# Kernel optimization log

Measured on AMD Instinct MI355X. Metric: run time of the kernel, lower is better.

The kernel has to match this reference:

```python
import jax, jax.numpy as jnp
import numpy as np

DIM = 1024
NUM_HEADS = 16
HEAD_DIM = DIM // NUM_HEADS
SCALE = 1.0 / float(np.sqrt(HEAD_DIM))


def setup_inputs() -> dict:
    key = jax.random.key(0)
    ks = jax.random.split(key, 5)
    B, S = 2, 2048
    x = jax.random.normal(ks[0], (B, S, DIM), dtype=jnp.float32)
    qkv_w = jax.random.normal(ks[1], (3 * DIM, DIM), dtype=jnp.float32) * (1.0 / np.sqrt(DIM))
    qkv_b = jax.random.normal(ks[2], (3 * DIM,), dtype=jnp.float32) * 0.02
    proj_w = jax.random.normal(ks[3], (DIM, DIM), dtype=jnp.float32) * (1.0 / np.sqrt(DIM))
    proj_b = jax.random.normal(ks[4], (DIM,), dtype=jnp.float32) * 0.02
    return {"x": x, "qkv_w": qkv_w, "qkv_b": qkv_b, "proj_w": proj_w, "proj_b": proj_b}


def reference(x, qkv_w, qkv_b, proj_w, proj_b):
    B, S, _ = x.shape
    # qkv projection: (B,S,3*DIM) -> (3, B, H, S, Dh)
    qkv = x @ qkv_w.T + qkv_b
    qkv = qkv.reshape(B, S, 3, NUM_HEADS, HEAD_DIM).transpose(2, 0, 3, 1, 4)
    q, k, v = qkv[0], qkv[1], qkv[2]
    # scaled dot-product attention (full score matrix, as in the original)
    scores = jnp.einsum('bhqd,bhkd->bhqk', q, k) * SCALE
    attn = jax.nn.softmax(scores, axis=-1)
    out = jnp.einsum('bhqk,bhkd->bhqd', attn, v)  # (B,H,S,Dh)
    out = out.transpose(0, 2, 1, 3).reshape(B, S, DIM)
    return out @ proj_w.T + proj_b
```

## Files before the change

### kernel.cpp

```cpp
#include <hip/hip_runtime.h>

#define DIM_ 1024
#define NH_ 16
#define HD_ 64
#define B_ 2
#define S_ 2048
#define M_ (B_ * S_)
#define NQKV_ (3 * DIM_)

typedef __attribute__((ext_vector_type(8))) __bf16 bf16x8;
typedef __attribute__((ext_vector_type(4))) __bf16 bf16x4;
typedef __attribute__((ext_vector_type(4))) float f32x4;

__device__ __forceinline__ void gl_lds16(const void* g, void* l) {
  __builtin_amdgcn_global_load_lds(
      (__attribute__((address_space(1))) void*)const_cast<void*>(g),
      (__attribute__((address_space(3))) void*)l, 16, 0, 0);
}

#define N4_X 1048576
#define N4_W1 786432
#define N4_W2 262144
__global__ __launch_bounds__(256) void cast_all(const float* __restrict__ x,
                                                const float* __restrict__ w1,
                                                const float* __restrict__ w2,
                                                __bf16* __restrict__ xb,
                                                __bf16* __restrict__ w1b,
                                                __bf16* __restrict__ w2b) {
  int i = blockIdx.x * 256 + threadIdx.x;
  const int stride = gridDim.x * 256;
  for (; i < N4_X + N4_W1 + N4_W2; i += stride) {
    const float4* src;
    bf16x4* dst;
    int j;
    if (i < N4_X) { src = (const float4*)x; dst = (bf16x4*)xb; j = i; }
    else if (i < N4_X + N4_W1) { src = (const float4*)w1; dst = (bf16x4*)w1b; j = i - N4_X; }
    else { src = (const float4*)w2; dst = (bf16x4*)w2b; j = i - (N4_X + N4_W1); }
    float4 v = src[j];
    bf16x4 o;
    o[0] = (__bf16)v.x; o[1] = (__bf16)v.y; o[2] = (__bf16)v.z; o[3] = (__bf16)v.w;
    dst[j] = o;
  }
}

template <int MODE>
__global__ __launch_bounds__(256) void gemm_bt(const __bf16* __restrict__ A,
                                               const __bf16* __restrict__ Bw,
                                               const float* __restrict__ bias,
                                               __bf16* __restrict__ Qp, __bf16* __restrict__ Kp,
                                               __bf16* __restrict__ Vt, float* __restrict__ Cout) {
  constexpr int KD = 1024;
  __shared__ __bf16 As[128 * 64];
  __shared__ __bf16 Bs[128 * 64];
  const int tid = threadIdx.x;
  const int lane = tid & 63;
  const int wave = tid >> 6;
  const int quad = lane >> 4;
  const int r16 = lane & 15;
  const int wm = wave >> 1;
  const int wn = wave & 1;
  const int m0 = blockIdx.y * 128;
  const int n0 = blockIdx.x * 128;

  const f32x4 fz = {0.f, 0.f, 0.f, 0.f};
  f32x4 acc[4][4];
#pragma unroll
  for (int i = 0; i < 4; ++i)
#pragma unroll
    for (int j = 0; j < 4; ++j) acc[i][j] = fz;

  const __bf16* ga[4];
  const __bf16* gb[4];
  __bf16 *la[4], *lb[4];
#pragma unroll
  for (int i = 0; i < 4; ++i) {
    const int c = tid + i * 256;
    const int r = c >> 3, cc = c & 7;
    const int col = ((cc ^ (r & 7)) * 8);
    ga[i] = A + (size_t)(m0 + r) * KD + col;
    gb[i] = Bw + (size_t)(n0 + r) * KD + col;
    la[i] = &As[c * 8];
    lb[i] = &Bs[c * 8];
  }

  for (int kt = 0; kt < KD / 64; ++kt) {
    __syncthreads();
#pragma unroll
    for (int i = 0; i < 4; ++i) {
      gl_lds16(ga[i], la[i]); ga[i] += 64;
      gl_lds16(gb[i], lb[i]); gb[i] += 64;
    }
    __syncthreads();

    bf16x8 af[2][4], bfr[2][4];
#pragma unroll
    for (int sub = 0; sub < 2; ++sub) {
      const int ch = ((sub * 4 + quad) ^ (r16 & 7)) * 8;
#pragma unroll
      for (int mt = 0; mt < 4; ++mt)
        af[sub][mt] = *(const bf16x8*)&As[(wm * 64 + mt * 16 + r16) * 64 + ch];
#pragma unroll
      for (int nt = 0; nt < 4; ++nt)
        bfr[sub][nt] = *(const bf16x8*)&Bs[(wn * 64 + nt * 16 + r16) * 64 + ch];
    }
#pragma unroll
    for (int sub = 0; sub < 2; ++sub)
#pragma unroll
      for (int mt = 0; mt < 4; ++mt)
#pragma unroll
        for (int nt = 0; nt < 4; ++nt)
          acc[mt][nt] =
              __builtin_amdgcn_mfma_f32_16x16x32_bf16(af[sub][mt], bfr[sub][nt], acc[mt][nt], 0, 0, 0);
  }

  if (MODE == 0) {
#pragma unroll
    for (int nt = 0; nt < 4; ++nt) {
      const int n = n0 + wn * 64 + nt * 16 + r16;
      const int sel = n >> 10;
      const int h = (n >> 6) & 15;
      const int dh = n & 63;
      const float bs = bias[n];
      if (sel == 2) {
#pragma unroll
        for (int mt = 0; mt < 4; ++mt) {
          const int m = m0 + wm * 64 + mt * 16 + quad * 4;
          const int b = m >> 11;
          const int s = m & 2047;
          const int slot = (s & ~31) | (((s >> 2) & 3) << 3) | (((s >> 4) & 1) << 2);
          bf16x4 ov;
#pragma unroll
          for (int r = 0; r < 4; ++r) ov[r] = (__bf16)(acc[mt][nt][r] + bs);
          *(bf16x4*)&Vt[((size_t)((b * NH_ + h) * HD_ + dh)) * S_ + slot] = ov;
        }
      } else {
        __bf16* dst = (sel == 0) ? Qp : Kp;
        const float mul = (sel == 0) ? 0.18033688011112042f : 1.0f;
#pragma unroll
        for (int mt = 0; mt < 4; ++mt) {
#pragma unroll
          for (int r = 0; r < 4; ++r) {
            const int m = m0 + wm * 64 + mt * 16 + quad * 4 + r;
            const int b = m >> 11;
            const int s = m & 2047;
            dst[((size_t)((b * NH_ + h) * S_ + s)) * HD_ + dh] =
                (__bf16)((acc[mt][nt][r] + bs) * mul);
          }
        }
      }
    }
  } else {
#pragma unroll
    for (int nt = 0; nt < 4; ++nt) {
      const int n = n0 + wn * 64 + nt * 16 + r16;
      const float bs = bias[n];
#pragma unroll
      for (int mt = 0; mt < 4; ++mt) {
#pragma unroll
        for (int r = 0; r < 4; ++r) {
          const int m = m0 + wm * 64 + mt * 16 + quad * 4 + r;
          Cout[(size_t)m * DIM_ + n] = acc[mt][nt][r] + bs;
        }
      }
    }
  }
}

__global__ __launch_bounds__(256) void attn(const __bf16* __restrict__ Qp,
                                            const __bf16* __restrict__ Kp,
                                            const __bf16* __restrict__ Vtp,
                                            __bf16* __restrict__ ctx) {
  __shared__ __bf16 Ks[128 * 64];
  __shared__ __bf16 Vs[64 * 128];
  const int tid = threadIdx.x;
  const int lane = tid & 63;
  const int wave = tid >> 6;
  const int quad = lane >> 4;
  const int r16 = lane & 15;
  const int bh = blockIdx.y;
  const int q0 = blockIdx.x * 128;

  bf16x8 qf[2][2];
#pragma unroll
  for (int g = 0; g < 2; ++g) {
    const __bf16* qb = Qp + ((size_t)bh * S_ + q0 + wave * 32 + g * 16 + r16) * HD_;
    qf[g][0] = *(const bf16x8*)(qb + quad * 8);
    qf[g][1] = *(const bf16x8*)(qb + 32 + quad * 8);
  }

  const f32x4 fz = {0.f, 0.f, 0.f, 0.f};
  f32x4 o[2][4];
  float lsum[2] = {0.f, 0.f};
#pragma unroll
  for (int g = 0; g < 2; ++g)
#pragma unroll
    for (int d = 0; d < 4; ++d) o[g][d] = fz;

  const __bf16* gk[4];
  const __bf16* gv[4];
  __bf16 *lk[4], *lv[4];
#pragma unroll
  for (int i = 0; i < 4; ++i) {
    int c = tid + i * 256;
    int kr = c >> 3, kc = c & 7;
    gk[i] = Kp + ((size_t)bh * S_ + kr) * HD_ + ((kc ^ (kr & 7)) * 8);
    lk[i] = &Ks[c * 8];
    int vr = c >> 4, vc = c & 15;
    gv[i] = Vtp + ((size_t)bh * HD_ + vr) * S_ + ((vc ^ (vr & 15)) * 8);
    lv[i] = &Vs[c * 8];
  }

  for (int kt = 0; kt < S_ / 128; ++kt) {
    __syncthreads();
#pragma unroll
    for (int i = 0; i < 4; ++i) { gl_lds16(gk[i], lk[i]); gk[i] += 128 * HD_; }
#pragma unroll
    for (int i = 0; i < 4; ++i) { gl_lds16(gv[i], lv[i]); gv[i] += 128; }
    __syncthreads();

    f32x4 sa[2][8];
#pragma unroll
    for (int mt = 0; mt < 8; ++mt) {
      const int row = mt * 16 + r16;
      bf16x8 k0 = *(const bf16x8*)&Ks[row * 64 + ((quad ^ (row & 7)) * 8)];
      bf16x8 k1 = *(const bf16x8*)&Ks[row * 64 + (((4 + quad) ^ (row & 7)) * 8)];
#pragma unroll
      for (int g = 0; g < 2; ++g) {
        f32x4 t = fz;
        t = __builtin_amdgcn_mfma_f32_16x16x32_bf16(k0, qf[g][0], t, 0, 0, 0);
        t = __builtin_amdgcn_mfma_f32_16x16x32_bf16(k1, qf[g][1], t, 0, 0, 0);
        sa[g][mt] = t;
      }
    }

    bf16x8 pf[2][4];
#pragma unroll
    for (int g = 0; g < 2; ++g)
#pragma unroll
      for (int ks = 0; ks < 4; ++ks)
#pragma unroll
        for (int r = 0; r < 4; ++r) {
          float p0 = __builtin_amdgcn_exp2f(sa[g][2 * ks][r]);
          float p1 = __builtin_amdgcn_exp2f(sa[g][2 * ks + 1][r]);
          lsum[g] += p0 + p1;
          pf[g][ks][r] = (__bf16)p0;
          pf[g][ks][4 + r] = (__bf16)p1;
        }

#pragma unroll
    for (int ks = 0; ks < 4; ++ks)
#pragma unroll
      for (int dt = 0; dt < 4; ++dt) {
        const int row = dt * 16 + r16;
        bf16x8 va = *(const bf16x8*)&Vs[row * 128 + (((4 * ks + quad) ^ (row & 15)) * 8)];
#pragma unroll
        for (int g = 0; g < 2; ++g)
          o[g][dt] = __builtin_amdgcn_mfma_f32_16x16x32_bf16(va, pf[g][ks], o[g][dt], 0, 0, 0);
      }
  }

  const int b = bh >> 4, h = bh & 15;
#pragma unroll
  for (int g = 0; g < 2; ++g) {
    float l = lsum[g];
    l += __shfl_xor(l, 16);
    l += __shfl_xor(l, 32);
    const float inv = 1.0f / l;
    const int s = q0 + wave * 32 + g * 16 + r16;
#pragma unroll
    for (int dt = 0; dt < 4; ++dt) {
      bf16x4 ov;
#pragma unroll
      for (int r = 0; r < 4; ++r) ov[r] = (__bf16)(o[g][dt][r] * inv);
      *(bf16x4*)&ctx[((size_t)(b * S_ + s)) * DIM_ + h * 64 + dt * 16 + quad * 4] = ov;
    }
  }
}

extern "C" void kernel_launch(void* const* d_in, const int* in_sizes, int n_in, void* d_out,
                              int out_size, void* d_ws, size_t ws_size, hipStream_t stream) {
  const float* x = (const float*)d_in[0];
  const float* qkv_w = (const float*)d_in[1];
  const float* qkv_b = (const float*)d_in[2];
  const float* proj_w = (const float*)d_in[3];
  const float* proj_b = (const float*)d_in[4];
  float* out = (float*)d_out;

  char* ws = (char*)d_ws;
  __bf16* Xb = (__bf16*)(ws);
  __bf16* Wb = (__bf16*)(ws + 8388608);
  __bf16* Pb = (__bf16*)(ws + 14680064);
  __bf16* Qp = (__bf16*)(ws + 16777216);
  __bf16* Kp = (__bf16*)(ws + 25165824);
  __bf16* Vt = (__bf16*)(ws + 33554432);
  __bf16* Cx = (__bf16*)(ws + 41943040);

  cast_all<<<2048, 256, 0, stream>>>(x, qkv_w, proj_w, Xb, Wb, Pb);
  gemm_bt<0><<<dim3(NQKV_ / 128, M_ / 128), 256, 0, stream>>>(Xb, Wb, qkv_b, Qp, Kp, Vt, nullptr);
  attn<<<dim3(S_ / 128, 32), 256, 0, stream>>>(Qp, Kp, Vt, Cx);
  gemm_bt<1><<<dim3(DIM_ / 128, M_ / 128), 256, 0, stream>>>(Cx, Pb, proj_b, nullptr, nullptr,
                                                             nullptr, out);
}
```

Baseline: 188.1 us.

## Double-buffer K/V tiles in attention and use 8 waves of 16 query rows

The attention kernel now uses two LDS buffers for K and V. It prefetches the next 128-key tile with global_load_lds while computing on the current one, and drops one of the two barriers per iteration. The block grows from 256 to 512 threads, so each wave handles 16 query rows instead of 32. This cuts per-thread registers and adds waves to hide latency. LDS use doubles to 64KB per block, which can limit how many blocks fit on a CU at once.

```diff
diff --git a/kernel.cpp b/kernel.cpp
--- a/kernel.cpp
+++ b/kernel.cpp
@@ -166,12 +166,12 @@
   }
 }
 
-__global__ __launch_bounds__(256) void attn(const __bf16* __restrict__ Qp,
+__global__ __launch_bounds__(512) void attn(const __bf16* __restrict__ Qp,
                                             const __bf16* __restrict__ Kp,
                                             const __bf16* __restrict__ Vtp,
                                             __bf16* __restrict__ ctx) {
-  __shared__ __bf16 Ks[128 * 64];
-  __shared__ __bf16 Vs[64 * 128];
+  __shared__ __bf16 Ks[2][128 * 64];
+  __shared__ __bf16 Vs[2][64 * 128];
   const int tid = threadIdx.x;
   const int lane = tid & 63;
   const int wave = tid >> 6;
@@ -179,101 +179,93 @@
   const int r16 = lane & 15;
   const int bh = blockIdx.y;
   const int q0 = blockIdx.x * 128;
-
-  bf16x8 qf[2][2];
-#pragma unroll
-  for (int g = 0; g < 2; ++g) {
-    const __bf16* qb = Qp + ((size_t)bh * S_ + q0 + wave * 32 + g * 16 + r16) * HD_;
-    qf[g][0] = *(const bf16x8*)(qb + quad * 8);
-    qf[g][1] = *(const bf16x8*)(qb + 32 + quad * 8);
-  }
+  const int qrow = q0 + wave * 16 + r16;
+
+  const __bf16* qb = Qp + ((size_t)bh * S_ + qrow) * HD_;
+  const bf16x8 qf0 = *(const bf16x8*)(qb + quad * 8);
+  const bf16x8 qf1 = *(const bf16x8*)(qb + 32 + quad * 8);
 
   const f32x4 fz = {0.f, 0.f, 0.f, 0.f};
-  f32x4 o[2][4];
-  float lsum[2] = {0.f, 0.f};
-#pragma unroll
-  for (int g = 0; g < 2; ++g)
-#pragma unroll
-    for (int d = 0; d < 4; ++d) o[g][d] = fz;
-
-  const __bf16* gk[4];
-  const __bf16* gv[4];
-  __bf16 *lk[4], *lv[4];
-#pragma unroll
-  for (int i = 0; i < 4; ++i) {
-    int c = tid + i * 256;
-    int kr = c >> 3, kc = c & 7;
+  f32x4 o[4];
+#pragma unroll
+  for (int d = 0; d < 4; ++d) o[d] = fz;
+  float lsum = 0.f;
+
+  const __bf16* gk[2];
+  const __bf16* gv[2];
+  int lofs[2];
+#pragma unroll
+  for (int i = 0; i < 2; ++i) {
+    const int c = tid + i * 512;
+    const int kr = c >> 3, kc = c & 7;
     gk[i] = Kp + ((size_t)bh * S_ + kr) * HD_ + ((kc ^ (kr & 7)) * 8);
-    lk[i] = &Ks[c * 8];
-    int vr = c >> 4, vc = c & 15;
+    const int vr = c >> 4, vc = c & 15;
     gv[i] = Vtp + ((size_t)bh * HD_ + vr) * S_ + ((vc ^ (vr & 15)) * 8);
-    lv[i] = &Vs[c * 8];
+    lofs[i] = c * 8;
+  }
+
+#pragma unroll
+  for (int i = 0; i < 2; ++i) {
+    gl_lds16(gk[i], &Ks[0][lofs[i]]); gk[i] += 128 * HD_;
+    gl_lds16(gv[i], &Vs[0][lofs[i]]); gv[i] += 128;
   }
 
   for (int kt = 0; kt < S_ / 128; ++kt) {
+    const int cb = kt & 1;
     __syncthreads();
-#pragma unroll
-    for (int i = 0; i < 4; ++i) { gl_lds16(gk[i], lk[i]); gk[i] += 128 * HD_; }
-#pragma unroll
-    for (int i = 0; i < 4; ++i) { gl_lds16(gv[i], lv[i]); gv[i] += 128; }
-    __syncthreads();
-
-    f32x4 sa[2][8];
+    if (kt + 1 < S_ / 128) {
+#pragma unroll
+      for (int i = 0; i < 2; ++i) {
+        gl_lds16(gk[i], &Ks[cb ^ 1][lofs[i]]); gk[i] += 128 * HD_;
+        gl_lds16(gv[i], &Vs[cb ^ 1][lofs[i]]); gv[i] += 128;
+      }
+    }
+
+    f32x4 sa[8];
 #pragma unroll
     for (int mt = 0; mt < 8; ++mt) {
       const int row = mt * 16 + r16;
-      bf16x8 k0 = *(const bf16x8*)&Ks[row * 64 + ((quad ^ (row & 7)) * 8)];
-      bf16x8 k1 = *(const bf16x8*)&Ks[row * 64 + (((4 + quad) ^ (row & 7)) * 8)];
-#pragma unroll
-      for (int g = 0; g < 2; ++g) {
-        f32x4 t = fz;
-        t = __builtin_amdgcn_mfma_f32_16x16x32_bf16(k0, qf[g][0], t, 0, 0, 0);
-        t = __builtin_amdgcn_mfma_f32_16x16x32_bf16(k1, qf[g][1], t, 0, 0, 0);
-        sa[g][mt] = t;
-      }
-    }
-
-    bf16x8 pf[2][4];
-#pragma unroll
-    for (int g = 0; g < 2; ++g)
-#pragma unroll
-      for (int ks = 0; ks < 4; ++ks)
-#pragma unroll
-        for (int r = 0; r < 4; ++r) {
-          float p0 = __builtin_amdgcn_exp2f(sa[g][2 * ks][r]);
-          float p1 = __builtin_amdgcn_exp2f(sa[g][2 * ks + 1][r]);
-          lsum[g] += p0 + p1;
-          pf[g][ks][r] = (__bf16)p0;
-          pf[g][ks][4 + r] = (__bf16)p1;
-        }
+      bf16x8 k0 = *(const bf16x8*)&Ks[cb][row * 64 + ((quad ^ (row & 7)) * 8)];
+      bf16x8 k1 = *(const bf16x8*)&Ks[cb][row * 64 + (((4 + quad) ^ (row & 7)) * 8)];
+      f32x4 t = fz;
+      t = __builtin_amdgcn_mfma_f32_16x16x32_bf16(k0, qf0, t, 0, 0, 0);
+      t = __builtin_amdgcn_mfma_f32_16x16x32_bf16(k1, qf1, t, 0, 0, 0);
+      sa[mt] = t;
+    }
+
+    bf16x8 pf[4];
+#pragma unroll
+    for (int ks = 0; ks < 4; ++ks)
+#pragma unroll
+      for (int r = 0; r < 4; ++r) {
+        float p0 = __builtin_amdgcn_exp2f(sa[2 * ks][r]);
+        float p1 = __builtin_amdgcn_exp2f(sa[2 * ks + 1][r]);
+        lsum += p0 + p1;
+        pf[ks][r] = (__bf16)p0;
+        pf[ks][4 + r] = (__bf16)p1;
+      }
 
 #pragma unroll
     for (int ks = 0; ks < 4; ++ks)
 #pragma unroll
       for (int dt = 0; dt < 4; ++dt) {
         const int row = dt * 16 + r16;
-        bf16x8 va = *(const bf16x8*)&Vs[row * 128 + (((4 * ks + quad) ^ (row & 15)) * 8)];
-#pragma unroll
-        for (int g = 0; g < 2; ++g)
-          o[g][dt] = __builtin_amdgcn_mfma_f32_16x16x32_bf16(va, pf[g][ks], o[g][dt], 0, 0, 0);
-      }
-  }
-
+        bf16x8 va = *(const bf16x8*)&Vs[cb][row * 128 + (((4 * ks + quad) ^ (row & 15)) * 8)];
+        o[dt] = __builtin_amdgcn_mfma_f32_16x16x32_bf16(va, pf[ks], o[dt], 0, 0, 0);
+      }
+  }
+
+  lsum += __shfl_xor(lsum, 16);
+  lsum += __shfl_xor(lsum, 32);
+  const float inv = 1.0f / lsum;
   const int b = bh >> 4, h = bh & 15;
-#pragma unroll
-  for (int g = 0; g < 2; ++g) {
-    float l = lsum[g];
-    l += __shfl_xor(l, 16);
-    l += __shfl_xor(l, 32);
-    const float inv = 1.0f / l;
-    const int s = q0 + wave * 32 + g * 16 + r16;
-#pragma unroll
-    for (int dt = 0; dt < 4; ++dt) {
-      bf16x4 ov;
-#pragma unroll
-      for (int r = 0; r < 4; ++r) ov[r] = (__bf16)(o[g][dt][r] * inv);
-      *(bf16x4*)&ctx[((size_t)(b * S_ + s)) * DIM_ + h * 64 + dt * 16 + quad * 4] = ov;
-    }
+  const int s = q0 + wave * 16 + r16;
+#pragma unroll
+  for (int dt = 0; dt < 4; ++dt) {
+    bf16x4 ov;
+#pragma unroll
+    for (int r = 0; r < 4; ++r) ov[r] = (__bf16)(o[dt][r] * inv);
+    *(bf16x4*)&ctx[((size_t)(b * S_ + s)) * DIM_ + h * 64 + dt * 16 + quad * 4] = ov;
   }
 }
 
@@ -297,7 +289,7 @@
 
   cast_all<<<2048, 256, 0, stream>>>(x, qkv_w, proj_w, Xb, Wb, Pb);
   gemm_bt<0><<<dim3(NQKV_ / 128, M_ / 128), 256, 0, stream>>>(Xb, Wb, qkv_b, Qp, Kp, Vt, nullptr);
-  attn<<<dim3(S_ / 128, 32), 256, 0, stream>>>(Qp, Kp, Vt, Cx);
+  attn<<<dim3(S_ / 128, 32), 512, 0, stream>>>(Qp, Kp, Vt, Cx);
   gemm_bt<1><<<dim3(DIM_ / 128, M_ / 128), 256, 0, stream>>>(Cx, Pb, proj_b, nullptr, nullptr,
                                                              nullptr, out);
 }
```

Result: no change. 186.0 us (-1.1%).
